# Performance work log

Measured on AMD Instinct MI355X. Metric: run time of the kernel, lower is better.

## Reference

```python
import jax, jax.numpy as jnp
import numpy as np

TOPK = 20
BN_EPS = 1e-5
NEG_SLOPE = 0.2  # DGL GAT default leaky_relu slope


def setup_inputs() -> dict:
    B, N, Ft, D = 128, 512, 64, 64
    key = jax.random.key(0)
    ks = jax.random.split(key, 6)
    return {
        "data": jax.random.normal(ks[0], (B, N, Ft), jnp.float32),
        "emb": jax.random.normal(ks[1], (N, D), jnp.float32) * 0.5,
        "fc_w": jax.random.normal(ks[2], (D, Ft), jnp.float32) * (1.0 / np.sqrt(Ft)),
        "fc_b": jnp.zeros((D,), jnp.float32),
        "attn_w": jax.random.normal(ks[3], (4 * D,), jnp.float32) * (1.0 / np.sqrt(4 * D)),
        "attn_b": jnp.zeros((), jnp.float32),
        "bn_gamma": jnp.ones((D,), jnp.float32),
        "bn_beta": jnp.zeros((D,), jnp.float32),
        "out_w": jax.random.normal(ks[4], (D,), jnp.float32) * (1.0 / np.sqrt(D)),
        "out_b": jnp.zeros((), jnp.float32),
    }


def reference(data, emb, fc_w, fc_b, attn_w, attn_b, bn_gamma, bn_beta, out_w, out_b):
    B, N, Ft = data.shape
    D = emb.shape[-1]

    # --- dynamic graph build from detached embeddings (cosine-sim topk) ---
    w = jax.lax.stop_gradient(emb)
    nrm = jnp.linalg.norm(w, axis=-1)
    cos = (w @ w.T) / (nrm[:, None] * nrm[None, :])      # [N, N]
    _, topk_idx = jax.lax.top_k(cos, TOPK)               # [N, TOPK]
    src = topk_idx.reshape(-1)                           # gated_j (message sources)
    dst = jnp.tile(jnp.arange(N), TOPK)                  # gated_i = arange(N).repeat(1,topk).flatten()

    # --- GAT layer: z = W x + b ; edge score from concat([z, emb]) at both ends ---
    z = jnp.einsum("bnf,df->bnd", data, fc_w) + fc_b     # [B, N, D]
    key_feat = jnp.concatenate([z, jnp.broadcast_to(emb, (B, N, D))], axis=-1)  # [B, N, 2D]
    a_src, a_dst = attn_w[: 2 * D], attn_w[2 * D :]
    s_src = jnp.einsum("bnd,d->bn", key_feat, a_src)
    s_dst = jnp.einsum("bnd,d->bn", key_feat, a_dst)
    e = jax.nn.leaky_relu(s_src[:, src] + s_dst[:, dst] + attn_b, NEG_SLOPE)    # [B, E]

    # segment softmax over incoming edges of each dst node (same edges every batch)
    m = jnp.full((B, N), -jnp.inf, e.dtype).at[:, dst].max(e)
    p = jnp.exp(e - m[:, dst])
    denom = jnp.zeros((B, N), e.dtype).at[:, dst].add(p)
    alpha = p / denom[:, dst]                            # [B, E]

    # scatter-aggregate messages
    h = jnp.zeros_like(z).at[:, dst].add(alpha[..., None] * z[:, src])          # [B, N, D]

    # --- trailing dense: mul by embedding, BatchNorm1d over channel D, relu, linear ---
    rst = h * emb[None]                                  # [B, N, D]
    mu = rst.mean(axis=(0, 1))
    var = rst.var(axis=(0, 1))
    rst = jax.nn.relu((rst - mu) / jnp.sqrt(var + BN_EPS) * bn_gamma + bn_beta)
    out = jnp.einsum("bnd,d->bn", rst, out_w) + out_b    # [B, N]
    return out
```

## Files before the change

### kernel.cpp

```cpp
#include <hip/hip_runtime.h>

#define NN 512
#define DD 64
#define TOPK 20
#define BB 128

__global__ __launch_bounds__(256) void k1_pre(const float* __restrict__ data,
                                              const float* __restrict__ emb,
                                              const float* __restrict__ fc_w,
                                              const float* __restrict__ fc_b,
                                              const float* __restrict__ attn_w,
                                              float* __restrict__ es_src,
                                              float* __restrict__ es_dst,
                                              double* __restrict__ gstats,
                                              float* __restrict__ z,
                                              float* __restrict__ zsrc,
                                              float* __restrict__ zdst,
                                              int* __restrict__ topk) {
    __shared__ __align__(16) char smem[34816];
    const int bid = blockIdx.x, t = threadIdx.x;

    if (bid < 512) {
        const int i = bid;
        double* cosrow = (double*)smem;
        double* nrmv   = (double*)(smem + 4096);
        float4* A4     = (float4*)(smem + 8192);
        const float4* e4 = (const float4*)emb;

        if (t < 16) A4[t] = e4[i * 16 + t];
        __syncthreads();

        #pragma unroll
        for (int jj = 0; jj < 2; ++jj) {
            const int j = jj * 256 + t;
            double dot = 0.0, ss = 0.0;
            #pragma unroll
            for (int c = 0; c < 16; ++c) {
                const float4 a = A4[c];
                const float4 b = e4[j * 16 + c];
                dot += (double)a.x * (double)b.x;
                dot += (double)a.y * (double)b.y;
                dot += (double)a.z * (double)b.z;
                dot += (double)a.w * (double)b.w;
                const double vx = b.x, vy = b.y, vz = b.z, vw = b.w;
                ss += vx * vx; ss += vy * vy; ss += vz * vz; ss += vw * vw;
            }
            cosrow[j] = dot;
            nrmv[j]   = sqrt(ss);
        }
        __syncthreads();

        if (t < 64) {
            const int lane = t;
            const double nrm_i = nrmv[i];
            double v[8];
            #pragma unroll
            for (int s = 0; s < 8; ++s)
                v[s] = cosrow[s * 64 + lane] / (nrm_i * nrmv[s * 64 + lane]);

            for (int k = 0; k < TOPK; ++k) {
                double bv = v[0]; int bs = 0;
                #pragma unroll
                for (int s = 1; s < 8; ++s) if (v[s] > bv) { bv = v[s]; bs = s; }
                int bi2 = bs * 64 + lane;
                #pragma unroll
                for (int off = 32; off > 0; off >>= 1) {
                    double ov = __shfl_xor(bv, off);
                    int    oi = __shfl_xor(bi2, off);
                    if (ov > bv || (ov == bv && oi < bi2)) { bv = ov; bi2 = oi; }
                }
                if (lane == 0) topk[i * TOPK + k] = bi2;
                const int  vsel = bi2 >> 6;
                const bool hit  = (bi2 & 63) == lane;
                #pragma unroll
                for (int s = 0; s < 8; ++s)
                    v[s] = (hit && vsel == s) ? -1e300 : v[s];
            }
        }
    } else if (bid < 1536) {
        float (*As)[68]  = (float(*)[68])smem;
        float (*WsT)[68] = (float(*)[68])(smem + 17408);
        const long r0 = (long)(bid - 512) * 64;
        const float4* data4 = (const float4*)data;
        const float4* fcw4  = (const float4*)fc_w;

        for (int m = t; m < 1024; m += 256) {
            const int r = m >> 4, c4 = m & 15;
            *(float4*)&As[r][c4 * 4] = data4[(r0 + r) * 16 + c4];
        }
        for (int m = t; m < 1024; m += 256) {
            const int d = m >> 4, f4 = m & 15;
            float4 v = fcw4[d * 16 + f4];
            WsT[f4 * 4 + 0][d] = v.x;
            WsT[f4 * 4 + 1][d] = v.y;
            WsT[f4 * 4 + 2][d] = v.z;
            WsT[f4 * 4 + 3][d] = v.w;
        }
        __syncthreads();

        const int tr = t >> 4, tc = t & 15;
        float acc[4][4] = {};
        for (int k0 = 0; k0 < 64; k0 += 4) {
            float4 a4[4], b4[4];
            #pragma unroll
            for (int i = 0; i < 4; ++i) a4[i] = *(float4*)&As[tr * 4 + i][k0];
            #pragma unroll
            for (int kk = 0; kk < 4; ++kk) b4[kk] = *(float4*)&WsT[k0 + kk][tc * 4];
            #pragma unroll
            for (int i = 0; i < 4; ++i) {
                acc[i][0] += a4[i].x * b4[0].x + a4[i].y * b4[1].x + a4[i].z * b4[2].x + a4[i].w * b4[3].x;
                acc[i][1] += a4[i].x * b4[0].y + a4[i].y * b4[1].y + a4[i].z * b4[2].y + a4[i].w * b4[3].y;
                acc[i][2] += a4[i].x * b4[0].z + a4[i].y * b4[1].z + a4[i].z * b4[2].z + a4[i].w * b4[3].z;
                acc[i][3] += a4[i].x * b4[0].w + a4[i].y * b4[1].w + a4[i].z * b4[2].w + a4[i].w * b4[3].w;
            }
        }
        float bias[4], aw0[4], aw2[4];
        #pragma unroll
        for (int j = 0; j < 4; ++j) {
            bias[j] = fc_b[tc * 4 + j];
            aw0[j]  = attn_w[tc * 4 + j];
            aw2[j]  = attn_w[128 + tc * 4 + j];
        }
        float zb[4][4];
        #pragma unroll
        for (int i = 0; i < 4; ++i) {
            #pragma unroll
            for (int j = 0; j < 4; ++j) zb[i][j] = acc[i][j] + bias[j];
            float4 vv; vv.x = zb[i][0]; vv.y = zb[i][1]; vv.z = zb[i][2]; vv.w = zb[i][3];
            *(float4*)&z[(r0 + tr * 4 + i) * 64 + tc * 4] = vv;
        }
        __syncthreads();

        float (*redA)[17] = (float(*)[17])smem;
        float (*redB)[17] = (float(*)[17])(smem + 4352);
        #pragma unroll
        for (int i = 0; i < 4; ++i) {
            redA[tr * 4 + i][tc] = zb[i][0] * aw0[0] + zb[i][1] * aw0[1] + zb[i][2] * aw0[2] + zb[i][3] * aw0[3];
            redB[tr * 4 + i][tc] = zb[i][0] * aw2[0] + zb[i][1] * aw2[1] + zb[i][2] * aw2[2] + zb[i][3] * aw2[3];
        }
        __syncthreads();
        if (t < 64) {
            float sA = 0.f, sB = 0.f;
            #pragma unroll
            for (int k = 0; k < 16; ++k) { sA += redA[t][k]; sB += redB[t][k]; }
            zsrc[r0 + t] = sA;
            zdst[r0 + t] = sB;
        }
    } else {
        #pragma unroll
        for (int jj = 0; jj < 2; ++jj) {
            const int j = jj * 256 + t;
            float s1 = 0.f, s2 = 0.f;
            #pragma unroll
            for (int c = 0; c < 64; ++c) {
                const float w = emb[j * 64 + c];
                s1 += w * attn_w[64 + c];
                s2 += w * attn_w[192 + c];
            }
            es_src[j] = s1;
            es_dst[j] = s2;
        }
        if (t < 128) gstats[t] = 0.0;
    }
}

__global__ __launch_bounds__(256) void k3_attn(const float* __restrict__ z,
                                               const float* __restrict__ zsrc,
                                               const float* __restrict__ zdst,
                                               const float* __restrict__ es_src,
                                               const float* __restrict__ es_dst,
                                               const int* __restrict__ topk,
                                               const float* __restrict__ emb,
                                               const float* __restrict__ attn_b_p,
                                               float* __restrict__ rst,
                                               double* __restrict__ gstats) {
    __shared__ float  zs[512 * 20];
    __shared__ double alf_pool[2560];
    __shared__ unsigned short sIdx[256 * 20];
    float* alf = (float*)alf_pool;
    const float4* alf4 = (const float4*)alf_pool;

    const int b    = blockIdx.x >> 2;
    const int dq   = blockIdx.x & 3;
    const int doff = dq * 16;
    const int t    = threadIdx.x;
    const float attn_b = *attn_b_p;
    const long b512 = (long)b * NN;

    float4* zs4 = (float4*)zs;
    for (int m = t; m < 2048; m += 256) {
        const int n = m >> 2, c4i = m & 3;
        zs4[n * 5 + c4i] = *(const float4*)(z + (b512 + n) * 64 + doff + c4i * 4);
    }
    __syncthreads();

    const int c4 = t & 3;
    const int rq = t >> 2;
    double s1[4] = {0,0,0,0}, s2[4] = {0,0,0,0};

    for (int chunk = 0; chunk < 2; ++chunk) {
        {
            const int n = chunk * 256 + t;
            const float sd = zdst[b512 + n] + es_dst[n] + attn_b;
            float ev[TOPK];
            float m0 = -1e30f;
            #pragma unroll
            for (int tt = 0; tt < TOPK; ++tt) {
                const int s = topk[n + tt * NN];
                sIdx[t * TOPK + tt] = (unsigned short)s;
                float e = zsrc[b512 + s] + es_src[s] + sd;
                e = (e >= 0.f) ? e : 0.2f * e;
                ev[tt] = e;
                m0 = fmaxf(m0, e);
            }
            float dsum = 0.f;
            #pragma unroll
            for (int tt = 0; tt < TOPK; ++tt) { ev[tt] = __expf(ev[tt] - m0); dsum += ev[tt]; }
            const float inv = 1.0f / dsum;
            #pragma unroll
            for (int tt = 0; tt < TOPK; ++tt) alf[t * TOPK + tt] = ev[tt] * inv;
        }
        __syncthreads();

        #pragma unroll
        for (int it = 0; it < 4; ++it) {
            const int nl = it * 64 + rq;
            const int n  = chunk * 256 + nl;
            float4 af[5];
            #pragma unroll
            for (int q = 0; q < 5; ++q) af[q] = alf4[nl * 5 + q];
            const float* av = (const float*)af;
            float4 acc = {0.f, 0.f, 0.f, 0.f};
            #pragma unroll
            for (int tt = 0; tt < TOPK; ++tt) {
                const float a = av[tt];
                const float4 zv = zs4[(int)sIdx[nl * TOPK + tt] * 5 + c4];
                acc.x += a * zv.x; acc.y += a * zv.y; acc.z += a * zv.z; acc.w += a * zv.w;
            }
            const float4 ev = *(const float4*)&emb[n * 64 + doff + c4 * 4];
            float4 r;
            r.x = acc.x * ev.x; r.y = acc.y * ev.y; r.z = acc.z * ev.z; r.w = acc.w * ev.w;
            *(float4*)&rst[(b512 + n) * 64 + doff + c4 * 4] = r;
            s1[0] += (double)r.x; s2[0] += (double)r.x * (double)r.x;
            s1[1] += (double)r.y; s2[1] += (double)r.y * (double)r.y;
            s1[2] += (double)r.z; s2[2] += (double)r.z * (double)r.z;
            s1[3] += (double)r.w; s2[3] += (double)r.w * (double)r.w;
        }
        __syncthreads();
    }

    double* r1 = alf_pool;
    double* r2 = alf_pool + 1024;
    #pragma unroll
    for (int j = 0; j < 4; ++j) {
        r1[(c4 * 4 + j) * 64 + rq] = s1[j];
        r2[(c4 * 4 + j) * 64 + rq] = s2[j];
    }
    __syncthreads();
    if (t < 16) {
        double a = 0.0, bb = 0.0;
        for (int q = 0; q < 64; ++q) { a += r1[t * 64 + q]; bb += r2[t * 64 + q]; }
        atomicAdd(&gstats[doff + t], a);
        atomicAdd(&gstats[64 + doff + t], bb);
    }
}

__global__ __launch_bounds__(256) void k5_out(const float* __restrict__ rst,
                                              const double* __restrict__ gstats,
                                              const float* __restrict__ gamma,
                                              const float* __restrict__ beta,
                                              const float* __restrict__ out_w,
                                              const float* __restrict__ out_b_p,
                                              float* __restrict__ out) {
    __shared__ float scv[64], biv[64];
    const int t = threadIdx.x;
    if (t < 64) {
        const double M = (double)BB * (double)NN;
        const double s  = gstats[t];
        const double s2 = gstats[64 + t];
        const double mu  = s / M;
        const double var = s2 / M - mu * mu;
        const float scale = (float)((double)gamma[t] / sqrt(var + 1e-5));
        scv[t] = scale;
        biv[t] = beta[t] - (float)mu * scale;
    }
    __syncthreads();

    const int wid = t >> 6, lane = t & 63;
    const float sc = scv[lane], bi = biv[lane], ow = out_w[lane];
    const float ob = *out_b_p;
    const long rowbase = (long)blockIdx.x * 16 + wid * 4;
    float v[4];
    #pragma unroll
    for (int rr = 0; rr < 4; ++rr)
        v[rr] = fmaxf(rst[(rowbase + rr) * 64 + lane] * sc + bi, 0.f) * ow;
    #pragma unroll
    for (int off = 32; off > 0; off >>= 1)
        #pragma unroll
        for (int rr = 0; rr < 4; ++rr) v[rr] += __shfl_down(v[rr], off);
    if (lane == 0)
        #pragma unroll
        for (int rr = 0; rr < 4; ++rr) out[rowbase + rr] = v[rr] + ob;
}

extern "C" void kernel_launch(void* const* d_in, const int* in_sizes, int n_in,
                              void* d_out, int out_size, void* d_ws, size_t ws_size,
                              hipStream_t stream) {
    const float* data   = (const float*)d_in[0];
    const float* emb    = (const float*)d_in[1];
    const float* fc_w   = (const float*)d_in[2];
    const float* fc_b   = (const float*)d_in[3];
    const float* attn_w = (const float*)d_in[4];
    const float* attn_b = (const float*)d_in[5];
    const float* gamma  = (const float*)d_in[6];
    const float* beta   = (const float*)d_in[7];
    const float* out_w  = (const float*)d_in[8];
    const float* out_b  = (const float*)d_in[9];
    float* out = (float*)d_out;

    char* ws = (char*)d_ws;
    float*  z      = (float*) (ws + 0);
    float*  rst    = (float*) (ws + 16777216);
    float*  zsrc   = (float*) (ws + 33554432);
    float*  zdst   = (float*) (ws + 33816576);
    int*    topk   = (int*)   (ws + 34078720);
    float*  es_src = (float*) (ws + 34119680);
    float*  es_dst = (float*) (ws + 34121728);
    double* gstats = (double*)(ws + 34123776);

    k1_pre<<<1537, 256, 0, stream>>>(data, emb, fc_w, fc_b, attn_w,
                                     es_src, es_dst, gstats,
                                     z, zsrc, zdst, topk);
    k3_attn<<<BB * 4, 256, 0, stream>>>(z, zsrc, zdst, es_src, es_dst, topk, emb,
                                        attn_b, rst, gstats);
    k5_out<<<4096, 256, 0, stream>>>(rst, gstats, gamma, beta, out_w, out_b, out);
}
```

Baseline: 135.9 us.

## Split top-k selection into its own fp32 kernel with shared-memory panel reuse

Moves the cosine-similarity top-k graph build out of the fused preprocessing kernel into a separate kernel. Each block now handles four rows, reusing a shared-memory panel of the embedding. All arithmetic uses fp32 instead of fp64, and each row's norm is folded into a single divide. The GEMM part becomes its own launch with 1025 blocks. The change cuts slow double-precision work and redundant global loads, but fp32 may flip near-tied top-k indices, and it adds one extra kernel launch.

```diff
diff --git a/kernel.cpp b/kernel.cpp
--- a/kernel.cpp
+++ b/kernel.cpp
@@ -5,82 +5,83 @@
 #define TOPK 20
 #define BB 128
 
-__global__ __launch_bounds__(256) void k1_pre(const float* __restrict__ data,
-                                              const float* __restrict__ emb,
-                                              const float* __restrict__ fc_w,
-                                              const float* __restrict__ fc_b,
-                                              const float* __restrict__ attn_w,
-                                              float* __restrict__ es_src,
-                                              float* __restrict__ es_dst,
-                                              double* __restrict__ gstats,
-                                              float* __restrict__ z,
-                                              float* __restrict__ zsrc,
-                                              float* __restrict__ zdst,
-                                              int* __restrict__ topk) {
+__global__ __launch_bounds__(256) void ksel(const float* __restrict__ emb,
+                                            int* __restrict__ topk) {
+    __shared__ __align__(16) float panel[128 * 68];
+    __shared__ __align__(16) float Arow[4 * 64];
+    const int t = threadIdx.x;
+    const int i0 = blockIdx.x * 4;
+    const int w = t >> 6, lane = t & 63;
+
+    Arow[t] = emb[i0 * 64 + t];
+
+    const float4* e4 = (const float4*)emb;
+    float4* p4 = (float4*)panel;
+    float v[8];
+
+    for (int p = 0; p < 4; ++p) {
+        __syncthreads();
+        for (int m = t; m < 2048; m += 256) {
+            const int r = m >> 4, c = m & 15;
+            p4[r * 17 + c] = e4[(p * 128 + r) * 16 + c];
+        }
+        __syncthreads();
+
+        #pragma unroll
+        for (int half = 0; half < 2; ++half) {
+            const int r = half * 64 + lane;
+            float dot = 0.f, ss = 0.f;
+            #pragma unroll
+            for (int c = 0; c < 16; ++c) {
+                const float4 b = p4[r * 17 + c];
+                const float4 a = *(const float4*)&Arow[w * 64 + c * 4];
+                dot += a.x * b.x; dot += a.y * b.y; dot += a.z * b.z; dot += a.w * b.w;
+                ss  += b.x * b.x; ss  += b.y * b.y; ss  += b.z * b.z; ss  += b.w * b.w;
+            }
+            v[p * 2 + half] = dot / sqrtf(ss);
+        }
+    }
+
+    int keep = 0;
+    for (int k = 0; k < TOPK; ++k) {
+        float bv = v[0]; int bs = 0;
+        #pragma unroll
+        for (int s = 1; s < 8; ++s) if (v[s] > bv) { bv = v[s]; bs = s; }
+        int bi2 = bs * 64 + lane;
+        #pragma unroll
+        for (int off = 32; off > 0; off >>= 1) {
+            float ov = __shfl_xor(bv, off);
+            int   oi = __shfl_xor(bi2, off);
+            if (ov > bv || (ov == bv && oi < bi2)) { bv = ov; bi2 = oi; }
+        }
+        if (lane == k) keep = bi2;
+        const int  vsel = bi2 >> 6;
+        const bool hit  = (bi2 & 63) == lane;
+        #pragma unroll
+        for (int s = 0; s < 8; ++s)
+            v[s] = (hit && vsel == s) ? -3.0e38f : v[s];
+    }
+    if (lane < TOPK) topk[(i0 + w) * TOPK + lane] = keep;
+}
+
+__global__ __launch_bounds__(256) void kgemm(const float* __restrict__ data,
+                                             const float* __restrict__ emb,
+                                             const float* __restrict__ fc_w,
+                                             const float* __restrict__ fc_b,
+                                             const float* __restrict__ attn_w,
+                                             float* __restrict__ es_src,
+                                             float* __restrict__ es_dst,
+                                             double* __restrict__ gstats,
+                                             float* __restrict__ z,
+                                             float* __restrict__ zsrc,
+                                             float* __restrict__ zdst) {
     __shared__ __align__(16) char smem[34816];
     const int bid = blockIdx.x, t = threadIdx.x;
 
-    if (bid < 512) {
-        const int i = bid;
-        double* cosrow = (double*)smem;
-        double* nrmv   = (double*)(smem + 4096);
-        float4* A4     = (float4*)(smem + 8192);
-        const float4* e4 = (const float4*)emb;
-
-        if (t < 16) A4[t] = e4[i * 16 + t];
-        __syncthreads();
-
-        #pragma unroll
-        for (int jj = 0; jj < 2; ++jj) {
-            const int j = jj * 256 + t;
-            double dot = 0.0, ss = 0.0;
-            #pragma unroll
-            for (int c = 0; c < 16; ++c) {
-                const float4 a = A4[c];
-                const float4 b = e4[j * 16 + c];
-                dot += (double)a.x * (double)b.x;
-                dot += (double)a.y * (double)b.y;
-                dot += (double)a.z * (double)b.z;
-                dot += (double)a.w * (double)b.w;
-                const double vx = b.x, vy = b.y, vz = b.z, vw = b.w;
-                ss += vx * vx; ss += vy * vy; ss += vz * vz; ss += vw * vw;
-            }
-            cosrow[j] = dot;
-            nrmv[j]   = sqrt(ss);
-        }
-        __syncthreads();
-
-        if (t < 64) {
-            const int lane = t;
-            const double nrm_i = nrmv[i];
-            double v[8];
-            #pragma unroll
-            for (int s = 0; s < 8; ++s)
-                v[s] = cosrow[s * 64 + lane] / (nrm_i * nrmv[s * 64 + lane]);
-
-            for (int k = 0; k < TOPK; ++k) {
-                double bv = v[0]; int bs = 0;
-                #pragma unroll
-                for (int s = 1; s < 8; ++s) if (v[s] > bv) { bv = v[s]; bs = s; }
-                int bi2 = bs * 64 + lane;
-                #pragma unroll
-                for (int off = 32; off > 0; off >>= 1) {
-                    double ov = __shfl_xor(bv, off);
-                    int    oi = __shfl_xor(bi2, off);
-                    if (ov > bv || (ov == bv && oi < bi2)) { bv = ov; bi2 = oi; }
-                }
-                if (lane == 0) topk[i * TOPK + k] = bi2;
-                const int  vsel = bi2 >> 6;
-                const bool hit  = (bi2 & 63) == lane;
-                #pragma unroll
-                for (int s = 0; s < 8; ++s)
-                    v[s] = (hit && vsel == s) ? -1e300 : v[s];
-            }
-        }
-    } else if (bid < 1536) {
+    if (bid < 1024) {
         float (*As)[68]  = (float(*)[68])smem;
         float (*WsT)[68] = (float(*)[68])(smem + 17408);
-        const long r0 = (long)(bid - 512) * 64;
+        const long r0 = (long)bid * 64;
         const float4* data4 = (const float4*)data;
         const float4* fcw4  = (const float4*)fc_w;
 
@@ -328,9 +329,9 @@
     float*  es_dst = (float*) (ws + 34121728);
     double* gstats = (double*)(ws + 34123776);
 
-    k1_pre<<<1537, 256, 0, stream>>>(data, emb, fc_w, fc_b, attn_w,
-                                     es_src, es_dst, gstats,
-                                     z, zsrc, zdst, topk);
+    ksel<<<128, 256, 0, stream>>>(emb, topk);
+    kgemm<<<1025, 256, 0, stream>>>(data, emb, fc_w, fc_b, attn_w,
+                                    es_src, es_dst, gstats, z, zsrc, zdst);
     k3_attn<<<BB * 4, 256, 0, stream>>>(z, zsrc, zdst, es_src, es_dst, topk, emb,
                                         attn_b, rst, gstats);
     k5_out<<<4096, 256, 0, stream>>>(rst, gstats, gamma, beta, out_w, out_b, out);
```

After: 147.7 us. +8.6%, slower.

## Replace double-precision iterative top-k with float keys and bitonic sort

Applied to the files above, without the earlier changes.

The cosine-similarity row is now computed in fp32 and divided only by the candidate's norm, since the row's own norm does not affect ranking. Each score is packed with its inverted index into a 64-bit sortable key. A full 512-element bitonic sort in shared memory across all 256 threads replaces the 64-lane, 20-iteration argmax loop. This removes slow FP64 arithmetic and the serial shuffle reductions, but adds many barriers, and fp32 rounding can flip near-tied neighbours.

```diff
diff --git a/kernel.cpp b/kernel.cpp
--- a/kernel.cpp
+++ b/kernel.cpp
@@ -22,60 +22,45 @@
 
     if (bid < 512) {
         const int i = bid;
-        double* cosrow = (double*)smem;
-        double* nrmv   = (double*)(smem + 4096);
-        float4* A4     = (float4*)(smem + 8192);
+        unsigned long long* keys = (unsigned long long*)smem;
+        float* Arow = (float*)(smem + 4096);
         const float4* e4 = (const float4*)emb;
 
-        if (t < 16) A4[t] = e4[i * 16 + t];
+        if (t < 64) Arow[t] = emb[i * 64 + t];
         __syncthreads();
 
         #pragma unroll
         for (int jj = 0; jj < 2; ++jj) {
             const int j = jj * 256 + t;
-            double dot = 0.0, ss = 0.0;
+            float dot = 0.f, ss = 0.f;
             #pragma unroll
             for (int c = 0; c < 16; ++c) {
-                const float4 a = A4[c];
                 const float4 b = e4[j * 16 + c];
-                dot += (double)a.x * (double)b.x;
-                dot += (double)a.y * (double)b.y;
-                dot += (double)a.z * (double)b.z;
-                dot += (double)a.w * (double)b.w;
-                const double vx = b.x, vy = b.y, vz = b.z, vw = b.w;
-                ss += vx * vx; ss += vy * vy; ss += vz * vz; ss += vw * vw;
-            }
-            cosrow[j] = dot;
-            nrmv[j]   = sqrt(ss);
-        }
-        __syncthreads();
-
-        if (t < 64) {
-            const int lane = t;
-            const double nrm_i = nrmv[i];
-            double v[8];
-            #pragma unroll
-            for (int s = 0; s < 8; ++s)
-                v[s] = cosrow[s * 64 + lane] / (nrm_i * nrmv[s * 64 + lane]);
-
-            for (int k = 0; k < TOPK; ++k) {
-                double bv = v[0]; int bs = 0;
-                #pragma unroll
-                for (int s = 1; s < 8; ++s) if (v[s] > bv) { bv = v[s]; bs = s; }
-                int bi2 = bs * 64 + lane;
-                #pragma unroll
-                for (int off = 32; off > 0; off >>= 1) {
-                    double ov = __shfl_xor(bv, off);
-                    int    oi = __shfl_xor(bi2, off);
-                    if (ov > bv || (ov == bv && oi < bi2)) { bv = ov; bi2 = oi; }
-                }
-                if (lane == 0) topk[i * TOPK + k] = bi2;
-                const int  vsel = bi2 >> 6;
-                const bool hit  = (bi2 & 63) == lane;
-                #pragma unroll
-                for (int s = 0; s < 8; ++s)
-                    v[s] = (hit && vsel == s) ? -1e300 : v[s];
-            }
+                const float4 a = *(const float4*)&Arow[c * 4];
+                dot += a.x * b.x; dot += a.y * b.y; dot += a.z * b.z; dot += a.w * b.w;
+                ss  += b.x * b.x; ss  += b.y * b.y; ss  += b.z * b.z; ss  += b.w * b.w;
+            }
+            const float v = dot / sqrtf(ss);
+            unsigned u = __float_as_uint(v);
+            u ^= (u >> 31) ? 0xFFFFFFFFu : 0x80000000u;
+            keys[j] = ((unsigned long long)u << 32) | (unsigned)(~j);
+        }
+        __syncthreads();
+
+        for (int size = 2; size <= 512; size <<= 1) {
+            for (int stride = size >> 1; stride > 0; stride >>= 1) {
+                const int lo = ((t & ~(stride - 1)) << 1) | (t & (stride - 1));
+                const int hi = lo + stride;
+                const bool up = ((lo & size) == 0);
+                const unsigned long long a = keys[lo], b2 = keys[hi];
+                if ((a > b2) == up) { keys[lo] = b2; keys[hi] = a; }
+                __syncthreads();
+            }
+        }
+
+        if (t < TOPK) {
+            const unsigned lo32 = (unsigned)keys[511 - t];
+            topk[i * TOPK + t] = (int)(~lo32);
         }
     } else if (bid < 1536) {
         float (*As)[68]  = (float(*)[68])smem;
```

New measurement: 135.1 us, median of 3. No clear change (-0.6%).
